# Kernel optimization log

Hardware: AMD Instinct MI355X
Metric: run time of the kernel (lower is better)

Reference implementation:

```python
import jax, jax.numpy as jnp
import numpy as np

HIDDEN = 1024
B, S = 4, 2048


def setup_inputs() -> dict:
    key = jax.random.key(0)
    ks = jax.random.split(key, 9)
    scale = 1.0 / np.sqrt(HIDDEN)
    mk = lambda k: (jax.random.normal(k, (HIDDEN, HIDDEN), dtype=jnp.float32) * scale)
    return {
        "x": jax.random.normal(ks[0], (B, S, HIDDEN), dtype=jnp.float32),
        "Wq": mk(ks[1]), "bq": jnp.zeros((HIDDEN,), jnp.float32),
        "Wk": mk(ks[2]), "bk": jnp.zeros((HIDDEN,), jnp.float32),
        "Wv": mk(ks[3]), "bv": jnp.zeros((HIDDEN,), jnp.float32),
        "Wo": mk(ks[4]), "bo": jnp.zeros((HIDDEN,), jnp.float32),
    }


def reference(x, Wq, bq, Wk, bk, Wv, bv, Wo, bo):
    # Single-head attention over the full hidden dim (num_heads unused in source).
    # Linear(H,H): y = x @ W^T + b ; weights stored [out,in] torch-style.
    q = jnp.einsum("bsh,oh->bso", x, Wq) + bq  # [B,S,H]
    k = jnp.einsum("bsh,oh->bso", x, Wk) + bk
    v = jnp.einsum("bsh,oh->bso", x, Wv) + bv
    scores = jnp.einsum("bqh,bkh->bqk", q, k) / jnp.sqrt(jnp.float32(HIDDEN))
    attn = jax.nn.softmax(scores, axis=-1)  # dropout rate is 0.0 (eval-equivalent)
    ctx = jnp.einsum("bqk,bkh->bqh", attn, v)
    return jnp.einsum("bsh,oh->bso", ctx, Wo) + bo
```

## Files before the change

kernel.cpp:

```cpp
#include <hip/hip_runtime.h>

#define HID 1024
#define SEQ 2048
#define NB 4
#define BS 8192

typedef __attribute__((ext_vector_type(8))) short short8;
typedef __attribute__((ext_vector_type(8))) unsigned short ushort8;
typedef __attribute__((ext_vector_type(4))) float f32x4;

__device__ __forceinline__ float bf2f(unsigned short u) {
  unsigned int x = ((unsigned int)u) << 16;
  return __builtin_bit_cast(float, x);
}
__device__ __forceinline__ unsigned short f2bf(float f) {
  unsigned int x = __builtin_bit_cast(unsigned int, f);
  x = x + 0x7fffu + ((x >> 16) & 1u);
  return (unsigned short)(x >> 16);
}

#define GLOAD16(g, l)                                                          \
  __builtin_amdgcn_global_load_lds(                                            \
      (const __attribute__((address_space(1))) unsigned int*)(g),              \
      (__attribute__((address_space(3))) unsigned int*)(l), 16, 0, 0)

__global__ void cast_f32_to_bf16(const float* __restrict__ in,
                                 unsigned short* __restrict__ out, int n) {
  int i = (blockIdx.x * 256 + threadIdx.x) * 8;
  if (i >= n) return;
  f32x4 a = *(const f32x4*)(in + i);
  f32x4 b = *(const f32x4*)(in + i + 4);
  ushort8 o;
  o[0] = f2bf(a[0]); o[1] = f2bf(a[1]); o[2] = f2bf(a[2]); o[3] = f2bf(a[3]);
  o[4] = f2bf(b[0]); o[5] = f2bf(b[1]); o[6] = f2bf(b[2]); o[7] = f2bf(b[3]);
  *(ushort8*)(out + i) = o;
}

__global__ __launch_bounds__(256) void transpose_cast(
    const float* __restrict__ in, unsigned short* __restrict__ out) {
  __shared__ float t[32][33];
  const int bx = blockIdx.x * 32, by = blockIdx.y * 32;
  const int tx = threadIdx.x & 31, ty = threadIdx.x >> 5;
#pragma unroll
  for (int i = 0; i < 4; ++i)
    t[ty + i * 8][tx] = in[(by + ty + i * 8) * 1024 + bx + tx];
  __syncthreads();
#pragma unroll
  for (int i = 0; i < 4; ++i)
    out[(bx + ty + i * 8) * 1024 + by + tx] = f2bf(t[tx][ty + i * 8]);
}

__global__ __launch_bounds__(256) void bias_fuse(const float* __restrict__ Wo,
                                                 const float* __restrict__ bv,
                                                 const float* __restrict__ bo,
                                                 float* __restrict__ bp) {
  const int row = blockIdx.x * 4 + (threadIdx.x >> 6);
  const int lane = threadIdx.x & 63;
  float s = 0.f;
  for (int k = lane; k < 1024; k += 64) s += Wo[row * 1024 + k] * bv[k];
#pragma unroll
  for (int off = 32; off >= 1; off >>= 1) s += __shfl_xor(s, off, 64);
  if (lane == 0) bp[row] = s + bo[row];
}

template <int BN, int OUT_F32, int BIAS_MODE>
__global__ __launch_bounds__(512, 2) void gemm2p(
    const unsigned short* __restrict__ A, const unsigned short* __restrict__ B,
    void* __restrict__ Cv, const float* __restrict__ bias,
    const float* __restrict__ bias2, int K, int lda, int ldb, int ldc,
    long long bsA, long long bsB, long long bsC, float alpha) {
  static_assert(BN == 256 || BN == 128, "BN");
  constexpr int WMW = (BN == 256) ? 2 : 4;
  constexpr int WNW = 8 / WMW;
  constexpr int MI = (256 / WMW) / 16;
  constexpr int GB = BN / 64;
  constexpr int WROWS = 256 / WMW;

  __shared__ unsigned short lA[2][256 * 64];
  __shared__ unsigned short lB[2][BN * 64];

  const int tid = threadIdx.x;
  const int lane = tid & 63, wid = tid >> 6;
  const int fr = lane & 15, fq = lane >> 4;
  const int wm = wid / WNW, wn = wid % WNW;

  const int nx = gridDim.x;
  const int nwg = nx * gridDim.y;
  int f = blockIdx.y * nx + blockIdx.x;
  f = (f & 7) * (nwg >> 3) + (f >> 3);
  const int bx = f % nx, by = f / nx;
  const int bz = blockIdx.z;

  const unsigned short* Ag = A + bz * bsA + (long long)by * 256 * lda;
  const unsigned short* Bg = B + bz * bsB + (long long)bx * BN * ldb;
  const int NT = K >> 6;

  const int srow = tid >> 3;
  const int gcol = 8 * ((tid & 7) ^ ((tid >> 3) & 7));
  const int ldst = wid * 512;

  auto stage = [&](int t) {
    const int b = t & 1;
#pragma unroll
    for (int c = 0; c < 4; ++c)
      GLOAD16(Ag + (long long)(c * 64 + srow) * lda + t * 64 + gcol,
              &lA[b][c * 4096 + ldst]);
#pragma unroll
    for (int c = 0; c < GB; ++c)
      GLOAD16(Bg + (long long)(c * 64 + srow) * ldb + t * 64 + gcol,
              &lB[b][c * 4096 + ldst]);
  };

  const int rxor = fr & 7;
  f32x4 acc[MI][4] = {};

  auto phase = [&](const unsigned short* pa, const unsigned short* pb,
                   int kk) {
    short8 av[MI], bw[4];
    const int slot = ((kk << 2) | fq) ^ rxor;
#pragma unroll
    for (int i = 0; i < MI; ++i)
      av[i] = *(const short8*)(pa + (wm * WROWS + i * 16 + fr) * 64 + slot * 8);
#pragma unroll
    for (int n = 0; n < 4; ++n)
      bw[n] = *(const short8*)(pb + (wn * 64 + n * 16 + fr) * 64 + slot * 8);
    asm volatile("s_waitcnt lgkmcnt(0)" ::: "memory");
    __builtin_amdgcn_sched_barrier(0);
    __builtin_amdgcn_s_setprio(1);
#pragma unroll
    for (int i = 0; i < MI; ++i)
#pragma unroll
      for (int n = 0; n < 4; ++n)
        acc[i][n] = __builtin_amdgcn_mfma_f32_16x16x32_bf16(av[i], bw[n],
                                                            acc[i][n], 0, 0, 0);
    __builtin_amdgcn_s_setprio(0);
  };

  stage(0);
  asm volatile("s_waitcnt vmcnt(0)" ::: "memory");
  __builtin_amdgcn_s_barrier();

  for (int t = 0; t < NT; ++t) {
    if (t + 1 < NT) stage(t + 1);
    const unsigned short* pa = lA[t & 1];
    const unsigned short* pb = lB[t & 1];
    phase(pa, pb, 0);
    phase(pa, pb, 1);
    asm volatile("s_waitcnt vmcnt(0)" ::: "memory");
    __builtin_amdgcn_s_barrier();
  }

  const long long cb0 = (long long)bz * bsC;
#pragma unroll
  for (int i = 0; i < MI; ++i)
#pragma unroll
    for (int j = 0; j < 4; ++j) {
      const int row = wm * WROWS + i * 16 + fq * 4 + j;
#pragma unroll
      for (int n = 0; n < 4; ++n) {
        const int col = bx * BN + wn * 64 + n * 16 + fr;
        float v = acc[i][n][j] * alpha;
        if (BIAS_MODE == 1) v += bias[col];
        if (BIAS_MODE == 3) v += (col < 1024) ? bias[col] : bias2[col - 1024];
        const long long idx = cb0 + (long long)(by * 256 + row) * ldc + col;
        if (OUT_F32)
          ((float*)Cv)[idx] = v;
        else
          ((unsigned short*)Cv)[idx] = f2bf(v);
      }
    }
}

template <int OUT_F32, int BIAS_MODE, int EPI>
__global__ __launch_bounds__(512, 4) void gemm_s(
    const unsigned short* __restrict__ A, const unsigned short* __restrict__ B,
    void* __restrict__ Cv, const float* __restrict__ bias,
    float* __restrict__ Srow, int K, int lda, int ldb, int ldc, long long bsA,
    long long bsB, long long bsC, float alpha) {
  __shared__ unsigned short lA[2][256 * 32];
  __shared__ unsigned short lB[2][128 * 32];

  const int tid = threadIdx.x;
  const int lane = tid & 63, wid = tid >> 6;
  const int fr = lane & 15, fq = lane >> 4;
  const int wm = wid >> 1, wn = wid & 1;

  const int nx = gridDim.x;
  const int nwg = nx * gridDim.y;
  int f = blockIdx.y * nx + blockIdx.x;
  f = (f & 7) * (nwg >> 3) + (f >> 3);
  const int bx = f % nx, by = f / nx;
  const int bz = blockIdx.z;

  const unsigned short* Ag = A + bz * bsA + (long long)by * 256 * lda;
  const unsigned short* Bg = B + bz * bsB + (long long)bx * 128 * ldb;
  const int NT = K >> 5;

  const int srow = tid >> 2;
  const int scol = 8 * ((tid & 3) ^ ((tid >> 3) & 3));
  const int ldst = wid * 512;

  auto stage = [&](int t) {
    const int b = t & 1;
    GLOAD16(Ag + (long long)srow * lda + t * 32 + scol, &lA[b][ldst]);
    GLOAD16(Ag + (long long)(128 + srow) * lda + t * 32 + scol,
            &lA[b][4096 + ldst]);
    GLOAD16(Bg + (long long)srow * ldb + t * 32 + scol, &lB[b][ldst]);
  };

  const int xm = ((fr >> 1) & 3) << 3;

  f32x4 acc[4][4] = {};

  stage(0);
  asm volatile("s_waitcnt vmcnt(0)" ::: "memory");
  __builtin_amdgcn_s_barrier();

  for (int t = 0; t < NT; ++t) {
    if (t + 1 < NT) stage(t + 1);
    const unsigned short* pa = lA[t & 1];
    const unsigned short* pb = lB[t & 1];
    short8 av[4], bw[4];
#pragma unroll
    for (int i = 0; i < 4; ++i)
      av[i] = *(const short8*)(pa +
                               (((wm * 64 + i * 16 + fr) * 32 + fq * 8) ^ xm));
#pragma unroll
    for (int n = 0; n < 4; ++n)
      bw[n] = *(const short8*)(pb +
                               (((wn * 64 + n * 16 + fr) * 32 + fq * 8) ^ xm));
    asm volatile("s_waitcnt lgkmcnt(0)" ::: "memory");
    __builtin_amdgcn_sched_barrier(0);
    __builtin_amdgcn_s_setprio(1);
#pragma unroll
    for (int i = 0; i < 4; ++i)
#pragma unroll
      for (int n = 0; n < 4; ++n)
        acc[i][n] = __builtin_amdgcn_mfma_f32_16x16x32_bf16(av[i], bw[n],
                                                            acc[i][n], 0, 0, 0);
    __builtin_amdgcn_s_setprio(0);
    asm volatile("s_waitcnt vmcnt(0)" ::: "memory");
    __builtin_amdgcn_s_barrier();
  }

  const long long cb0 = (long long)bz * bsC;
  float* sredf = (float*)lA;
#pragma unroll
  for (int i = 0; i < 4; ++i)
#pragma unroll
    for (int j = 0; j < 4; ++j) {
      const int row = wm * 64 + i * 16 + fq * 4 + j;
      float inv = 1.0f;
      if (EPI == 2) inv = 1.0f / Srow[(long long)bz * SEQ + by * 256 + row];
      float rps = 0.0f;
#pragma unroll
      for (int n = 0; n < 4; ++n) {
        const int col = bx * 128 + wn * 64 + n * 16 + fr;
        float v = acc[i][n][j] * alpha;
        if (EPI == 1) { v = __expf(v); rps += v; }
        if (EPI == 2) v *= inv;
        if (BIAS_MODE == 1) v += bias[col];
        const long long idx = cb0 + (long long)(by * 256 + row) * ldc + col;
        if (OUT_F32)
          ((float*)Cv)[idx] = v;
        else
          ((unsigned short*)Cv)[idx] = f2bf(v);
      }
      if (EPI == 1) {
        rps += __shfl_xor(rps, 1, 64);
        rps += __shfl_xor(rps, 2, 64);
        rps += __shfl_xor(rps, 4, 64);
        rps += __shfl_xor(rps, 8, 64);
        if (fr == 0) sredf[row * 2 + wn] = rps;
      }
    }
  if (EPI == 1) {
    __syncthreads();
    if (tid < 256) {
      const float s2 = sredf[tid * 2] + sredf[tid * 2 + 1];
      atomicAdd(Srow + (long long)bz * SEQ + by * 256 + tid, s2);
    }
  }
}

extern "C" void kernel_launch(void* const* d_in, const int* in_sizes, int n_in,
                              void* d_out, int out_size, void* d_ws,
                              size_t ws_size, hipStream_t stream) {
  (void)in_sizes; (void)n_in; (void)out_size; (void)ws_size;
  const float* x = (const float*)d_in[0];
  const float* Wq = (const float*)d_in[1];
  const float* bq = (const float*)d_in[2];
  const float* Wk = (const float*)d_in[3];
  const float* bk = (const float*)d_in[4];
  const float* Wv = (const float*)d_in[5];
  const float* bv = (const float*)d_in[6];
  const float* Wo = (const float*)d_in[7];
  const float* bo = (const float*)d_in[8];
  float* out = (float*)d_out;

  char* ws = (char*)d_ws;
  unsigned short* xbf  = (unsigned short*)(ws + 0);
  unsigned short* wqk  = (unsigned short*)(ws + 16777216);
  unsigned short* wobf = (unsigned short*)(ws + 20971520);
  unsigned short* wvT  = (unsigned short*)(ws + 23068672);
  unsigned short* wov  = (unsigned short*)(ws + 25165824);
  float*          bpr  = (float*)        (ws + 27262976);
  float*          Srow = (float*)        (ws + 28311552);
  unsigned short* VWoT = (unsigned short*)(ws + 33554432);
  unsigned short* QKb  = (unsigned short*)(ws + 50331648);
  unsigned short* P    = (unsigned short*)(ws + 83886080);

  cast_f32_to_bf16<<<4096, 256, 0, stream>>>(x, xbf, BS * HID);
  cast_f32_to_bf16<<<512, 256, 0, stream>>>(Wq, wqk, HID * HID);
  cast_f32_to_bf16<<<512, 256, 0, stream>>>(Wk, wqk + HID * HID, HID * HID);
  cast_f32_to_bf16<<<512, 256, 0, stream>>>(Wo, wobf, HID * HID);
  transpose_cast<<<dim3(32, 32), 256, 0, stream>>>(Wv, wvT);
  bias_fuse<<<256, 256, 0, stream>>>(Wo, bv, bo, bpr);
  hipMemsetAsync(Srow, 0, NB * SEQ * sizeof(float), stream);

  gemm2p<128, 0, 0><<<dim3(8, 4, 1), 512, 0, stream>>>(
      wobf, wvT, wov, nullptr, nullptr, HID, HID, HID, HID, 0, 0, 0, 1.0f);
  gemm2p<128, 0, 0><<<dim3(64, 4, 1), 512, 0, stream>>>(
      wov, xbf, VWoT, nullptr, nullptr, HID, HID, HID, BS, 0, 0, 0, 1.0f);
  gemm2p<256, 0, 3><<<dim3(8, 32, 1), 512, 0, stream>>>(
      xbf, wqk, QKb, bq, bk, HID, HID, HID, 2048, 0, 0, 0, 1.0f);
  gemm_s<0, 0, 1><<<dim3(16, 8, NB), 512, 0, stream>>>(
      QKb, QKb + 1024, P, nullptr, Srow, HID, 2048, 2048, SEQ,
      (long long)SEQ * 2048, (long long)SEQ * 2048, (long long)SEQ * SEQ,
      0.03125f);
  gemm_s<1, 1, 2><<<dim3(8, 8, NB), 512, 0, stream>>>(
      P, VWoT, out, bpr, Srow, SEQ, SEQ, BS, HID, (long long)SEQ * SEQ,
      (long long)SEQ, (long long)SEQ * HID, 1.0f);
}
```

Baseline: 224.0 us.

## Merge prep kernels into one launch and fuse QK/VWo projection GEMMs

```diff
diff --git a/kernel.cpp b/kernel.cpp
--- a/kernel.cpp
+++ b/kernel.cpp
@@ -24,43 +24,59 @@
       (const __attribute__((address_space(1))) unsigned int*)(g),              \
       (__attribute__((address_space(3))) unsigned int*)(l), 16, 0, 0)
 
-__global__ void cast_f32_to_bf16(const float* __restrict__ in,
-                                 unsigned short* __restrict__ out, int n) {
-  int i = (blockIdx.x * 256 + threadIdx.x) * 8;
-  if (i >= n) return;
-  f32x4 a = *(const f32x4*)(in + i);
-  f32x4 b = *(const f32x4*)(in + i + 4);
-  ushort8 o;
-  o[0] = f2bf(a[0]); o[1] = f2bf(a[1]); o[2] = f2bf(a[2]); o[3] = f2bf(a[3]);
-  o[4] = f2bf(b[0]); o[5] = f2bf(b[1]); o[6] = f2bf(b[2]); o[7] = f2bf(b[3]);
-  *(ushort8*)(out + i) = o;
-}
-
-__global__ __launch_bounds__(256) void transpose_cast(
-    const float* __restrict__ in, unsigned short* __restrict__ out) {
-  __shared__ float t[32][33];
-  const int bx = blockIdx.x * 32, by = blockIdx.y * 32;
-  const int tx = threadIdx.x & 31, ty = threadIdx.x >> 5;
-#pragma unroll
-  for (int i = 0; i < 4; ++i)
-    t[ty + i * 8][tx] = in[(by + ty + i * 8) * 1024 + bx + tx];
-  __syncthreads();
-#pragma unroll
-  for (int i = 0; i < 4; ++i)
-    out[(bx + ty + i * 8) * 1024 + by + tx] = f2bf(t[tx][ty + i * 8]);
-}
-
-__global__ __launch_bounds__(256) void bias_fuse(const float* __restrict__ Wo,
-                                                 const float* __restrict__ bv,
-                                                 const float* __restrict__ bo,
-                                                 float* __restrict__ bp) {
-  const int row = blockIdx.x * 4 + (threadIdx.x >> 6);
-  const int lane = threadIdx.x & 63;
-  float s = 0.f;
-  for (int k = lane; k < 1024; k += 64) s += Wo[row * 1024 + k] * bv[k];
-#pragma unroll
-  for (int off = 32; off >= 1; off >>= 1) s += __shfl_xor(s, off, 64);
-  if (lane == 0) bp[row] = s + bo[row];
+__global__ __launch_bounds__(256) void prep(
+    const float* __restrict__ x, const float* __restrict__ Wq,
+    const float* __restrict__ bq, const float* __restrict__ Wk,
+    const float* __restrict__ Wv, const float* __restrict__ bv,
+    const float* __restrict__ Wo, const float* __restrict__ bo,
+    unsigned short* __restrict__ xbf, unsigned short* __restrict__ wqk,
+    unsigned short* __restrict__ wobf, unsigned short* __restrict__ wvT,
+    float* __restrict__ bpr, float* __restrict__ Srow) {
+  const int blk = blockIdx.x;
+  const int tid = threadIdx.x;
+  if (blk < 4096) {
+    const long long i = ((long long)blk * 256 + tid) * 8;
+    f32x4 a = *(const f32x4*)(x + i);
+    f32x4 b = *(const f32x4*)(x + i + 4);
+    ushort8 o;
+    o[0] = f2bf(a[0]); o[1] = f2bf(a[1]); o[2] = f2bf(a[2]); o[3] = f2bf(a[3]);
+    o[4] = f2bf(b[0]); o[5] = f2bf(b[1]); o[6] = f2bf(b[2]); o[7] = f2bf(b[3]);
+    *(ushort8*)(xbf + i) = o;
+  } else if (blk < 5632) {
+    const float* src = (blk < 4608) ? Wq : (blk < 5120) ? Wk : Wo;
+    unsigned short* dst =
+        (blk < 4608) ? wqk : (blk < 5120) ? (wqk + HID * HID) : wobf;
+    const int b = (blk - 4096) & 511;
+    const int i = (b * 256 + tid) * 8;
+    f32x4 a = *(const f32x4*)(src + i);
+    f32x4 c = *(const f32x4*)(src + i + 4);
+    ushort8 o;
+    o[0] = f2bf(a[0]); o[1] = f2bf(a[1]); o[2] = f2bf(a[2]); o[3] = f2bf(a[3]);
+    o[4] = f2bf(c[0]); o[5] = f2bf(c[1]); o[6] = f2bf(c[2]); o[7] = f2bf(c[3]);
+    *(ushort8*)(dst + i) = o;
+  } else if (blk < 6656) {
+    __shared__ float t[32][33];
+    const int b = blk - 5632;
+    const int bx = (b & 31) * 32, by = (b >> 5) * 32;
+    const int tx = tid & 31, ty = tid >> 5;
+#pragma unroll
+    for (int i = 0; i < 4; ++i)
+      t[ty + i * 8][tx] = Wv[(by + ty + i * 8) * 1024 + bx + tx];
+    __syncthreads();
+#pragma unroll
+    for (int i = 0; i < 4; ++i)
+      wvT[(bx + ty + i * 8) * 1024 + by + tx] = f2bf(t[tx][ty + i * 8]);
+  } else if (blk < 6912) {
+    const int row = (blk - 6656) * 4 + (tid >> 6);
+    const int lane = tid & 63;
+    float s = 0.f;
+    for (int k = lane; k < 1024; k += 64) s += Wo[row * 1024 + k] * bv[k];
+#pragma unroll
+    for (int off = 32; off >= 1; off >>= 1) s += __shfl_xor(s, off, 64);
+    if (lane == 0) bpr[row] = s + bo[row];
+  } else {
+    Srow[(blk - 6912) * 256 + tid] = 0.0f;
+  }
 }
 
 template <int BN, int OUT_F32, int BIAS_MODE>
@@ -171,6 +187,103 @@
     }
 }
 
+__device__ __forceinline__ void gemm_core(
+    const unsigned short* __restrict__ A0, const unsigned short* __restrict__ B0,
+    unsigned short* __restrict__ C, const float* __restrict__ bias,
+    const float* __restrict__ bias2, int bias_mode, int K, int lda, int ldb,
+    int ldc, float alpha, int bid, int nx, int nwg,
+    unsigned short (&lA)[2][256 * 32], unsigned short (&lB)[2][128 * 32]) {
+  const int tid = threadIdx.x;
+  const int lane = tid & 63, wid = tid >> 6;
+  const int fr = lane & 15, fq = lane >> 4;
+  const int wm = wid >> 1, wn = wid & 1;
+
+  int f = (bid & 7) * (nwg >> 3) + (bid >> 3);
+  const int bx = f % nx, by = f / nx;
+
+  const unsigned short* Ag = A0 + (long long)by * 256 * lda;
+  const unsigned short* Bg = B0 + (long long)bx * 128 * ldb;
+  const int NT = K >> 5;
+
+  const int srow = tid >> 2;
+  const int scol = 8 * ((tid & 3) ^ ((tid >> 3) & 3));
+  const int ldst = wid * 512;
+
+  auto stage = [&](int t) {
+    const int b = t & 1;
+    GLOAD16(Ag + (long long)srow * lda + t * 32 + scol, &lA[b][ldst]);
+    GLOAD16(Ag + (long long)(128 + srow) * lda + t * 32 + scol,
+            &lA[b][4096 + ldst]);
+    GLOAD16(Bg + (long long)srow * ldb + t * 32 + scol, &lB[b][ldst]);
+  };
+
+  const int xm = ((fr >> 1) & 3) << 3;
+  f32x4 acc[4][4] = {};
+
+  stage(0);
+  asm volatile("s_waitcnt vmcnt(0)" ::: "memory");
+  __builtin_amdgcn_s_barrier();
+
+  for (int t = 0; t < NT; ++t) {
+    if (t + 1 < NT) stage(t + 1);
+    const unsigned short* pa = lA[t & 1];
+    const unsigned short* pb = lB[t & 1];
+    short8 av[4], bw[4];
+#pragma unroll
+    for (int i = 0; i < 4; ++i)
+      av[i] = *(const short8*)(pa +
+                               (((wm * 64 + i * 16 + fr) * 32 + fq * 8) ^ xm));
+#pragma unroll
+    for (int n = 0; n < 4; ++n)
+      bw[n] = *(const short8*)(pb +
+                               (((wn * 64 + n * 16 + fr) * 32 + fq * 8) ^ xm));
+    asm volatile("s_waitcnt lgkmcnt(0)" ::: "memory");
+    __builtin_amdgcn_sched_barrier(0);
+    __builtin_amdgcn_s_setprio(1);
+#pragma unroll
+    for (int i = 0; i < 4; ++i)
+#pragma unroll
+      for (int n = 0; n < 4; ++n)
+        acc[i][n] = __builtin_amdgcn_mfma_f32_16x16x32_bf16(av[i], bw[n],
+                                                            acc[i][n], 0, 0, 0);
+    __builtin_amdgcn_s_setprio(0);
+    asm volatile("s_waitcnt vmcnt(0)" ::: "memory");
+    __builtin_amdgcn_s_barrier();
+  }
+
+#pragma unroll
+  for (int i = 0; i < 4; ++i)
+#pragma unroll
+    for (int j = 0; j < 4; ++j) {
+      const int row = wm * 64 + i * 16 + fq * 4 + j;
+#pragma unroll
+      for (int n = 0; n < 4; ++n) {
+        const int col = bx * 128 + wn * 64 + n * 16 + fr;
+        float v = acc[i][n][j] * alpha;
+        if (bias_mode == 1) v += bias[col];
+        else if (bias_mode == 3) v += (col < 1024) ? bias[col] : bias2[col - 1024];
+        C[(long long)(by * 256 + row) * ldc + col] = f2bf(v);
+      }
+    }
+}
+
+__global__ __launch_bounds__(512, 4) void gemm_dual(
+    const unsigned short* __restrict__ xbf, const unsigned short* __restrict__ wqk,
+    const unsigned short* __restrict__ wov, unsigned short* __restrict__ QKb,
+    unsigned short* __restrict__ VWoT, const float* __restrict__ bq,
+    const float* __restrict__ bk) {
+  __shared__ unsigned short lA[2][256 * 32];
+  __shared__ unsigned short lB[2][128 * 32];
+  const int bid = blockIdx.x;
+  if (bid < 512) {
+    gemm_core(xbf, wqk, QKb, bq, bk, 3, HID, HID, HID, 2048, 1.0f, bid, 16,
+              512, lA, lB);
+  } else {
+    gemm_core(wov, xbf, VWoT, nullptr, nullptr, 0, HID, HID, HID, BS, 1.0f,
+              bid - 512, 64, 256, lA, lB);
+  }
+}
+
 template <int OUT_F32, int BIAS_MODE, int EPI>
 __global__ __launch_bounds__(512, 4) void gemm_s(
     const unsigned short* __restrict__ A, const unsigned short* __restrict__ B,
@@ -209,7 +322,6 @@
   };
 
   const int xm = ((fr >> 1) & 3) << 3;
-
   f32x4 acc[4][4] = {};
 
   stage(0);
@@ -310,20 +422,11 @@
   unsigned short* QKb  = (unsigned short*)(ws + 50331648);
   unsigned short* P    = (unsigned short*)(ws + 83886080);
 
-  cast_f32_to_bf16<<<4096, 256, 0, stream>>>(x, xbf, BS * HID);
-  cast_f32_to_bf16<<<512, 256, 0, stream>>>(Wq, wqk, HID * HID);
-  cast_f32_to_bf16<<<512, 256, 0, stream>>>(Wk, wqk + HID * HID, HID * HID);
-  cast_f32_to_bf16<<<512, 256, 0, stream>>>(Wo, wobf, HID * HID);
-  transpose_cast<<<dim3(32, 32), 256, 0, stream>>>(Wv, wvT);
-  bias_fuse<<<256, 256, 0, stream>>>(Wo, bv, bo, bpr);
-  hipMemsetAsync(Srow, 0, NB * SEQ * sizeof(float), stream);
-
+  prep<<<6944, 256, 0, stream>>>(x, Wq, bq, Wk, Wv, bv, Wo, bo, xbf, wqk,
+                                 wobf, wvT, bpr, Srow);
   gemm2p<128, 0, 0><<<dim3(8, 4, 1), 512, 0, stream>>>(
       wobf, wvT, wov, nullptr, nullptr, HID, HID, HID, HID, 0, 0, 0, 1.0f);
-  gemm2p<128, 0, 0><<<dim3(64, 4, 1), 512, 0, stream>>>(
-      wov, xbf, VWoT, nullptr, nullptr, HID, HID, HID, BS, 0, 0, 0, 1.0f);
-  gemm2p<256, 0, 3><<<dim3(8, 32, 1), 512, 0, stream>>>(
-      xbf, wqk, QKb, bq, bk, HID, HID, HID, 2048, 0, 0, 0, 1.0f);
+  gemm_dual<<<768, 512, 0, stream>>>(xbf, wqk, wov, QKb, VWoT, bq, bk);
   gemm_s<0, 0, 1><<<dim3(16, 8, NB), 512, 0, stream>>>(
       QKb, QKb + 1024, P, nullptr, Srow, HID, 2048, 2048, SEQ,
       (long long)SEQ * 2048, (long long)SEQ * 2048, (long long)SEQ * SEQ,
```

Result: faster. 212.9 us (-5.0%).
